# Kernel tuning notes

Measured on AMD Instinct MI355X. Metric: run time of the kernel, lower is better.

The kernel has to match this reference:

```python
import jax, jax.numpy as jnp
import numpy as np

N = 524288   # total samples
D = 128      # embedding dim
S = 128      # samples per group (equal-size contiguous groups)
G = N // S   # number of groups = 4096
MARGIN = 2.0
K_MARGIN = 0.02
EPS = 1e-6


def setup_inputs() -> dict:
    key = jax.random.key(0)
    k1, k2, k3, k4 = jax.random.split(key, 4)
    z_r = jax.random.normal(k1, (N, D), jnp.float32)
    z_v = jax.random.normal(k2, (N, D), jnp.float32)
    labels = jax.random.randint(k3, (N,), 0, 2, dtype=jnp.int32)
    # contiguous equal-size groups: group id = index // S
    groups = (jnp.arange(N, dtype=jnp.int32) // S).astype(jnp.int32)
    var_lens = jax.random.randint(k4, (N,), 0, 100, dtype=jnp.int32)
    return {"z_r": z_r, "z_v": z_v, "labels": labels, "groups": groups, "var_lens": var_lens}


def _std1(x):
    # torch.Tensor.std default is unbiased (ddof=1)
    return jnp.std(x, axis=1, ddof=1)


def reference(z_r, z_v, labels, groups, var_lens):
    # cosine distance per row: [N]
    d = 1.0 - jnp.sum(z_r * z_v, axis=-1)

    # ----- contrastive distance-difference loss -----
    mb = labels == 0
    mp = labels == 1
    nb = mb.sum()
    npos = mp.sum()
    mean_b = jnp.sum(jnp.where(mb, d, 0.0)) / jnp.maximum(nb, 1)
    mean_p = jnp.sum(jnp.where(mp, d, 0.0)) / jnp.maximum(npos, 1)
    l_cdd = jnp.where((nb > 0) & (npos > 0),
                      jax.nn.relu(MARGIN + mean_b - mean_p), 0.0)

    # ----- per-group losses, vectorized over groups as [G, S] -----
    # groups is arange(N)//S -> contiguous equal-size groups, so reshape is exact
    vlen = var_lens.reshape(G, S).astype(jnp.float32)
    dist = d.reshape(G, S)

    vs = _std1(vlen)   # [G]
    ds = _std1(dist)   # [G]
    vz = (vlen - vlen.mean(axis=1, keepdims=True)) / (vs[:, None] + EPS)
    dz = (dist - dist.mean(axis=1, keepdims=True)) / (ds[:, None] + EPS)
    corr_loss = jnp.where((vs > 0) & (ds > 0),
                          jnp.mean((vz - dz) ** 2, axis=1), 0.0)  # [G]

    order = jnp.argsort(vlen, axis=1)
    v_sorted = jnp.take_along_axis(vlen, order, axis=1)  # [G,S]
    d_sorted = jnp.take_along_axis(dist, order, axis=1)  # [G,S]

    neigh_viol = jnp.mean(
        jax.nn.relu(d_sorted[:, :-1] - d_sorted[:, 1:] + K_MARGIN), axis=1)  # [G]

    # pairwise diffs: dv[g,i,j] = v[g,j] - v[g,i] (torch unsqueeze(0)-unsqueeze(1))
    dv = v_sorted[:, None, :] - v_sorted[:, :, None]  # [G,S,S]
    dd = d_sorted[:, None, :] - d_sorted[:, :, None]  # [G,S,S]
    mask = dv > 0
    cnt = mask.sum(axis=(1, 2))  # [G]
    viol_sum = jnp.sum(jnp.where(mask, jax.nn.relu(K_MARGIN - dd), 0.0), axis=(1, 2))
    rank_loss = jnp.where(cnt > 0, viol_sum / jnp.maximum(cnt, 1), 0.0)  # [G]

    group_losses = corr_loss + neigh_viol + rank_loss  # [G]
    sizes = jnp.full((G,), float(S), jnp.float32)
    weights = sizes / sizes.sum()
    l_pcc = jnp.sum(weights * group_losses)

    return (l_cdd, l_pcc, d)
```

## Files before the change

### kernel.cpp

```cpp
#include <hip/hip_runtime.h>
#include <hip/hip_bf16.h>

#define D_DIM   128
#define S_GRP   128
#define MARGINF 2.0f
#define KMARG   0.02f
#define EPSF    1e-6f

#define CD_BLOCKS  1024
#define CD_THREADS 256
#define U_PAIRS    8

template <bool USE_PARTIALS>
__global__ __launch_bounds__(CD_THREADS) void compute_d_kernel(
    const float* __restrict__ zr, const float* __restrict__ zv,
    const int* __restrict__ labels, float* __restrict__ dout,
    float* __restrict__ partB, float* __restrict__ partP,
    int* __restrict__ pcntB, int* __restrict__ pcntP,
    double* __restrict__ wsd, int* __restrict__ wsi, int npairs)
{
    const int tid    = blockIdx.x * blockDim.x + threadIdx.x;
    const int wave   = tid >> 6;
    const int lane   = threadIdx.x & 63;
    const int nwaves = (gridDim.x * blockDim.x) >> 6;
    const int half   = lane >> 5;
    const int sub    = lane & 31;

    float accB = 0.f, accP = 0.f;
    int   cntB = 0,   cntP = 0;

    const int nchunks = npairs / U_PAIRS;

    for (int c = wave; c < nchunks; c += nwaves) {
        const int pair0 = c * U_PAIRS;
        float4 x[U_PAIRS], y[U_PAIRS];
        #pragma unroll
        for (int u = 0; u < U_PAIRS; ++u) {
            const size_t r = (size_t)(2 * (pair0 + u) + half);
            x[u] = ((const float4*)(zr + r * D_DIM))[sub];
            y[u] = ((const float4*)(zv + r * D_DIM))[sub];
        }
        float p[U_PAIRS];
        #pragma unroll
        for (int u = 0; u < U_PAIRS; ++u)
            p[u] = x[u].x * y[u].x + x[u].y * y[u].y
                 + x[u].z * y[u].z + x[u].w * y[u].w;
        #pragma unroll
        for (int off = 16; off; off >>= 1) {
            #pragma unroll
            for (int u = 0; u < U_PAIRS; ++u) p[u] += __shfl_xor(p[u], off);
        }
        if (sub == 0) {
            #pragma unroll
            for (int u = 0; u < U_PAIRS; ++u) {
                const int r = 2 * (pair0 + u) + half;
                const float dv = 1.0f - p[u];
                dout[r] = dv;
                if (labels[r] == 0) { accB += dv; cntB++; }
                else                { accP += dv; cntP++; }
            }
        }
    }

    #pragma unroll
    for (int off = 32; off; off >>= 1) {
        accB += __shfl_xor(accB, off);
        accP += __shfl_xor(accP, off);
        cntB += __shfl_xor(cntB, off);
        cntP += __shfl_xor(cntP, off);
    }
    __shared__ float sB[4], sP[4];
    __shared__ int   iB[4], iP[4];
    const int w = threadIdx.x >> 6;
    if (lane == 0) { sB[w] = accB; sP[w] = accP; iB[w] = cntB; iP[w] = cntP; }
    __syncthreads();
    if (threadIdx.x == 0) {
        const float tB = sB[0] + sB[1] + sB[2] + sB[3];
        const float tP = sP[0] + sP[1] + sP[2] + sP[3];
        const int   cB = iB[0] + iB[1] + iB[2] + iB[3];
        const int   cP = iP[0] + iP[1] + iP[2] + iP[3];
        if (USE_PARTIALS) {
            partB[blockIdx.x] = tB;
            partP[blockIdx.x] = tP;
            pcntB[blockIdx.x] = cB;
            pcntP[blockIdx.x] = cP;
        } else {
            atomicAdd(&wsd[0], (double)tB);
            atomicAdd(&wsd[1], (double)tP);
            atomicAdd(&wsi[0], cB);
            atomicAdd(&wsi[1], cP);
        }
    }
}

__device__ __forceinline__ float block_reduce_128(float x, volatile float* sh)
{
    #pragma unroll
    for (int off = 32; off; off >>= 1) x += __shfl_xor(x, off);
    __syncthreads();
    if ((threadIdx.x & 63) == 0) sh[threadIdx.x >> 6] = x;
    __syncthreads();
    return sh[0] + sh[1];
}

template <bool USE_PARTIALS>
__global__ __launch_bounds__(128) void group_kernel(
    const int* __restrict__ var_lens, const float* __restrict__ dvals,
    float* __restrict__ gl, double* __restrict__ pcc_sum)
{
    const int g = blockIdx.x;
    const int t = threadIdx.x;
    __shared__ float sv[S_GRP], sd[S_GRP], svs[S_GRP], sds[S_GRP];
    __shared__ float sred[2];

    const float v = (float)var_lens[(size_t)g * S_GRP + t];
    const float d = dvals[(size_t)g * S_GRP + t];
    sv[t] = v; sd[t] = d;

    const float mv = block_reduce_128(v, sred) * (1.0f / S_GRP);
    const float md = block_reduce_128(d, sred) * (1.0f / S_GRP);
    const float cv = v - mv, cd = d - md;

    const float ssv = block_reduce_128(cv * cv, sred);
    const float ssd = block_reduce_128(cd * cd, sred);
    const float vs  = sqrtf(ssv * (1.0f / (S_GRP - 1)));
    const float dsd = sqrtf(ssd * (1.0f / (S_GRP - 1)));

    const float vz = cv / (vs + EPSF);
    const float dz = cd / (dsd + EPSF);
    const float df = vz - dz;
    float corr = block_reduce_128(df * df, sred) * (1.0f / S_GRP);
    if (!(vs > 0.f && dsd > 0.f)) corr = 0.f;

    int rank = 0;
    #pragma unroll 8
    for (int j = 0; j < S_GRP; ++j) {
        const float vj = sv[j];
        rank += (vj < v) || (vj == v && j < t);
    }
    svs[rank] = v; sds[rank] = d;
    __syncthreads();

    float nv = 0.f;
    if (t < S_GRP - 1) nv = fmaxf(sds[t] - sds[t + 1] + KMARG, 0.f);
    const float neigh = block_reduce_128(nv, sred) * (1.0f / (S_GRP - 1));

    const float myv = svs[t], myd = sds[t];
    float viol = 0.f, cnt = 0.f;
    #pragma unroll 8
    for (int j = 0; j < S_GRP; ++j) {
        const float vj = svs[j];
        if (vj > myv) {
            cnt  += 1.f;
            viol += fmaxf(KMARG - (sds[j] - myd), 0.f);
        }
    }
    const float violT = block_reduce_128(viol, sred);
    const float cntT  = block_reduce_128(cnt,  sred);
    const float rloss = (cntT > 0.f) ? violT / cntT : 0.f;

    if (t == 0) {
        const float total = corr + neigh + rloss;
        if (USE_PARTIALS) gl[g] = total;
        else              atomicAdd(pcc_sum, (double)total);
    }
}

__global__ __launch_bounds__(256) void finalize_kernel(
    const float* __restrict__ partB, const float* __restrict__ partP,
    const int* __restrict__ pcntB, const int* __restrict__ pcntP,
    const float* __restrict__ gl, float* __restrict__ out,
    int nPart, int nGroups)
{
    double a0 = 0.0, a1 = 0.0, a2 = 0.0, a3 = 0.0, a4 = 0.0;
    for (int i = threadIdx.x; i < nPart; i += 256) {
        a0 += (double)partB[i];
        a1 += (double)partP[i];
        a2 += (double)pcntB[i];
        a3 += (double)pcntP[i];
    }
    for (int i = threadIdx.x; i < nGroups; i += 256)
        a4 += (double)gl[i];

    #pragma unroll
    for (int off = 32; off; off >>= 1) {
        a0 += __shfl_xor(a0, off);
        a1 += __shfl_xor(a1, off);
        a2 += __shfl_xor(a2, off);
        a3 += __shfl_xor(a3, off);
        a4 += __shfl_xor(a4, off);
    }
    __shared__ double red[5][4];
    const int w = threadIdx.x >> 6;
    if ((threadIdx.x & 63) == 0) {
        red[0][w] = a0; red[1][w] = a1; red[2][w] = a2; red[3][w] = a3; red[4][w] = a4;
    }
    __syncthreads();
    if (threadIdx.x == 0) {
        const double sB = red[0][0] + red[0][1] + red[0][2] + red[0][3];
        const double sP = red[1][0] + red[1][1] + red[1][2] + red[1][3];
        const double cB = red[2][0] + red[2][1] + red[2][2] + red[2][3];
        const double cP = red[3][0] + red[3][1] + red[3][2] + red[3][3];
        const double sG = red[4][0] + red[4][1] + red[4][2] + red[4][3];
        const double mean_b = sB / (cB > 0.0 ? cB : 1.0);
        const double mean_p = sP / (cP > 0.0 ? cP : 1.0);
        float l = 0.f;
        if (cB > 0.0 && cP > 0.0) {
            const double vv = (double)MARGINF + mean_b - mean_p;
            l = (float)(vv > 0.0 ? vv : 0.0);
        }
        out[0] = l;
        out[1] = (float)(sG / (double)nGroups);
    }
}

__global__ void finalize_atomic_kernel(const double* __restrict__ wsd,
                                       const int* __restrict__ wsi,
                                       float* __restrict__ out, int nGroups)
{
    if (threadIdx.x == 0 && blockIdx.x == 0) {
        const int nb = wsi[0], np_ = wsi[1];
        const double mean_b = wsd[0] / (double)(nb  > 0 ? nb  : 1);
        const double mean_p = wsd[1] / (double)(np_ > 0 ? np_ : 1);
        float l = 0.f;
        if (nb > 0 && np_ > 0) {
            const double v = (double)MARGINF + mean_b - mean_p;
            l = (float)(v > 0.0 ? v : 0.0);
        }
        out[0] = l;
        out[1] = (float)(wsd[2] / (double)nGroups);
    }
}

extern "C" void kernel_launch(void* const* d_in, const int* in_sizes, int n_in,
                              void* d_out, int out_size, void* d_ws, size_t ws_size,
                              hipStream_t stream)
{
    const float* zr       = (const float*)d_in[0];
    const float* zv       = (const float*)d_in[1];
    const int*   labels   = (const int*)d_in[2];
    const int*   var_lens = (const int*)d_in[4];
    float* out = (float*)d_out;

    const int N = in_sizes[2];
    const int G = N / S_GRP;

    const size_t need = (size_t)CD_BLOCKS * 16 + (size_t)G * 4;

    if (ws_size >= need) {
        float* partB = (float*)d_ws;
        float* partP = partB + CD_BLOCKS;
        int*   pcntB = (int*)(partP + CD_BLOCKS);
        int*   pcntP = pcntB + CD_BLOCKS;
        float* gl    = (float*)(pcntP + CD_BLOCKS);

        compute_d_kernel<true><<<CD_BLOCKS, CD_THREADS, 0, stream>>>(
            zr, zv, labels, out + 2, partB, partP, pcntB, pcntP,
            nullptr, nullptr, N / 2);
        group_kernel<true><<<G, 128, 0, stream>>>(var_lens, out + 2, gl, nullptr);
        finalize_kernel<<<1, 256, 0, stream>>>(partB, partP, pcntB, pcntP, gl,
                                               out, CD_BLOCKS, G);
    } else {
        double* wsd = (double*)d_ws;
        int*    wsi = (int*)((char*)d_ws + 3 * sizeof(double));
        hipMemsetAsync(d_ws, 0, 3 * sizeof(double) + 2 * sizeof(int), stream);

        compute_d_kernel<false><<<CD_BLOCKS, CD_THREADS, 0, stream>>>(
            zr, zv, labels, out + 2, nullptr, nullptr, nullptr, nullptr,
            wsd, wsi, N / 2);
        group_kernel<false><<<G, 128, 0, stream>>>(var_lens, out + 2, nullptr,
                                                   wsd + 2);
        finalize_atomic_kernel<<<1, 64, 0, stream>>>(wsd, wsi, out, G);
    }
}
```

Before: 552.6 us.

## Fuse distance computation into per-group kernel with double-buffered row loads

Merges the cosine-distance kernel and the per-group loss kernel into one kernel with one block per group. The block computes its 128 distances into LDS through a software-pipelined, double-buffered load of z_r/z_v rows, then runs the group statistics, and also emits per-group label sums for the contrastive loss. This removes a launch and the global write-then-reread of d between kernels. In exchange, the bandwidth-bound dot-product phase now runs with 128-thread blocks and carries the register pressure of the pipelined loads, and the finalize pass now reduces 4096 per-group partials instead of 1024 per-block ones.

After: 540.2 us. 2.2% less time.

```diff
diff --git a/kernel.cpp b/kernel.cpp
--- a/kernel.cpp
+++ b/kernel.cpp
@@ -1,5 +1,4 @@
 #include <hip/hip_runtime.h>
-#include <hip/hip_bf16.h>
 
 #define D_DIM   128
 #define S_GRP   128
@@ -7,92 +6,6 @@
 #define KMARG   0.02f
 #define EPSF    1e-6f
 
-#define CD_BLOCKS  1024
-#define CD_THREADS 256
-#define U_PAIRS    8
-
-template <bool USE_PARTIALS>
-__global__ __launch_bounds__(CD_THREADS) void compute_d_kernel(
-    const float* __restrict__ zr, const float* __restrict__ zv,
-    const int* __restrict__ labels, float* __restrict__ dout,
-    float* __restrict__ partB, float* __restrict__ partP,
-    int* __restrict__ pcntB, int* __restrict__ pcntP,
-    double* __restrict__ wsd, int* __restrict__ wsi, int npairs)
-{
-    const int tid    = blockIdx.x * blockDim.x + threadIdx.x;
-    const int wave   = tid >> 6;
-    const int lane   = threadIdx.x & 63;
-    const int nwaves = (gridDim.x * blockDim.x) >> 6;
-    const int half   = lane >> 5;
-    const int sub    = lane & 31;
-
-    float accB = 0.f, accP = 0.f;
-    int   cntB = 0,   cntP = 0;
-
-    const int nchunks = npairs / U_PAIRS;
-
-    for (int c = wave; c < nchunks; c += nwaves) {
-        const int pair0 = c * U_PAIRS;
-        float4 x[U_PAIRS], y[U_PAIRS];
-        #pragma unroll
-        for (int u = 0; u < U_PAIRS; ++u) {
-            const size_t r = (size_t)(2 * (pair0 + u) + half);
-            x[u] = ((const float4*)(zr + r * D_DIM))[sub];
-            y[u] = ((const float4*)(zv + r * D_DIM))[sub];
-        }
-        float p[U_PAIRS];
-        #pragma unroll
-        for (int u = 0; u < U_PAIRS; ++u)
-            p[u] = x[u].x * y[u].x + x[u].y * y[u].y
-                 + x[u].z * y[u].z + x[u].w * y[u].w;
-        #pragma unroll
-        for (int off = 16; off; off >>= 1) {
-            #pragma unroll
-            for (int u = 0; u < U_PAIRS; ++u) p[u] += __shfl_xor(p[u], off);
-        }
-        if (sub == 0) {
-            #pragma unroll
-            for (int u = 0; u < U_PAIRS; ++u) {
-                const int r = 2 * (pair0 + u) + half;
-                const float dv = 1.0f - p[u];
-                dout[r] = dv;
-                if (labels[r] == 0) { accB += dv; cntB++; }
-                else                { accP += dv; cntP++; }
-            }
-        }
-    }
-
-    #pragma unroll
-    for (int off = 32; off; off >>= 1) {
-        accB += __shfl_xor(accB, off);
-        accP += __shfl_xor(accP, off);
-        cntB += __shfl_xor(cntB, off);
-        cntP += __shfl_xor(cntP, off);
-    }
-    __shared__ float sB[4], sP[4];
-    __shared__ int   iB[4], iP[4];
-    const int w = threadIdx.x >> 6;
-    if (lane == 0) { sB[w] = accB; sP[w] = accP; iB[w] = cntB; iP[w] = cntP; }
-    __syncthreads();
-    if (threadIdx.x == 0) {
-        const float tB = sB[0] + sB[1] + sB[2] + sB[3];
-        const float tP = sP[0] + sP[1] + sP[2] + sP[3];
-        const int   cB = iB[0] + iB[1] + iB[2] + iB[3];
-        const int   cP = iP[0] + iP[1] + iP[2] + iP[3];
-        if (USE_PARTIALS) {
-            partB[blockIdx.x] = tB;
-            partP[blockIdx.x] = tP;
-            pcntB[blockIdx.x] = cB;
-            pcntP[blockIdx.x] = cP;
-        } else {
-            atomicAdd(&wsd[0], (double)tB);
-            atomicAdd(&wsd[1], (double)tP);
-            atomicAdd(&wsi[0], cB);
-            atomicAdd(&wsi[1], cP);
-        }
-    }
-}
-
 __device__ __forceinline__ float block_reduce_128(float x, volatile float* sh)
 {
     #pragma unroll
@@ -104,23 +17,95 @@
 }
 
 template <bool USE_PARTIALS>
-__global__ __launch_bounds__(128) void group_kernel(
-    const int* __restrict__ var_lens, const float* __restrict__ dvals,
-    float* __restrict__ gl, double* __restrict__ pcc_sum)
-{
-    const int g = blockIdx.x;
-    const int t = threadIdx.x;
-    __shared__ float sv[S_GRP], sd[S_GRP], svs[S_GRP], sds[S_GRP];
+__global__ __launch_bounds__(128, 4) void fused_kernel(
+    const float* __restrict__ zr, const float* __restrict__ zv,
+    const int* __restrict__ labels, const int* __restrict__ var_lens,
+    float* __restrict__ dout,
+    float* __restrict__ gl, float* __restrict__ pB, float* __restrict__ pP,
+    float* __restrict__ pcB, float* __restrict__ pcP,
+    double* __restrict__ wsd, int* __restrict__ wsi)
+{
+    const int g    = blockIdx.x;
+    const int t    = threadIdx.x;
+    const int w    = t >> 6;
+    const int lane = t & 63;
+    const int half = lane >> 5;
+    const int sub  = lane & 31;
+
+    __shared__ __align__(16) float sv[S_GRP], sd[S_GRP], svs[S_GRP], sds[S_GRP];
     __shared__ float sred[2];
 
-    const float v = (float)var_lens[(size_t)g * S_GRP + t];
-    const float d = dvals[(size_t)g * S_GRP + t];
-    sv[t] = v; sd[t] = d;
+    const int slabRow = g * S_GRP + w * 64;
+    const int ldsRow  = w * 64;
+
+    float4 XA[4], YA[4], XB[4], YB[4];
+
+#define LOAD8(X, Y, ls) do {                                                  \
+        const float* _bz = zr + (size_t)(slabRow + 8*(ls) + 4*half) * D_DIM;  \
+        const float* _bv = zv + (size_t)(slabRow + 8*(ls) + 4*half) * D_DIM;  \
+        _Pragma("unroll")                                                     \
+        for (int u = 0; u < 4; ++u) {                                         \
+            X[u] = ((const float4*)(_bz + (size_t)u * D_DIM))[sub];           \
+            Y[u] = ((const float4*)(_bv + (size_t)u * D_DIM))[sub];           \
+        } } while (0)
+
+#define DOT_STORE(X, Y, ls) do {                                              \
+        float _p[4];                                                          \
+        _Pragma("unroll")                                                     \
+        for (int u = 0; u < 4; ++u)                                           \
+            _p[u] = X[u].x*Y[u].x + X[u].y*Y[u].y                             \
+                  + X[u].z*Y[u].z + X[u].w*Y[u].w;                            \
+        _Pragma("unroll")                                                     \
+        for (int off = 16; off; off >>= 1) {                                  \
+            _Pragma("unroll")                                                 \
+            for (int u = 0; u < 4; ++u) _p[u] += __shfl_xor(_p[u], off);      \
+        }                                                                     \
+        if (sub == 0) {                                                       \
+            const float4 _dv = make_float4(1.f - _p[0], 1.f - _p[1],          \
+                                           1.f - _p[2], 1.f - _p[3]);         \
+                      \
+            float* _dp = dout + (size_t)(slabRow + 8*(ls)) + 4*half;          \
+            ((float2*)_dp)[0] = make_float2(_dv.x, _dv.y);                    \
+            ((float2*)_dp)[1] = make_float2(_dv.z, _dv.w);                    \
+            ((float4*)sd)[((ldsRow + 8*(ls)) >> 2) + half] = _dv;             \
+        } } while (0)
+
+    LOAD8(XA, YA, 0);
+    LOAD8(XB, YB, 1);
+    DOT_STORE(XA, YA, 0);
+    LOAD8(XA, YA, 2);
+    DOT_STORE(XB, YB, 1);
+    LOAD8(XB, YB, 3);
+    DOT_STORE(XA, YA, 2);
+    LOAD8(XA, YA, 4);
+    DOT_STORE(XB, YB, 3);
+    LOAD8(XB, YB, 5);
+    DOT_STORE(XA, YA, 4);
+    LOAD8(XA, YA, 6);
+    DOT_STORE(XB, YB, 5);
+    LOAD8(XB, YB, 7);
+    DOT_STORE(XA, YA, 6);
+    DOT_STORE(XB, YB, 7);
+
+#undef LOAD8
+#undef DOT_STORE
+
+    __syncthreads();
+
+    const float v   = (float)var_lens[(size_t)g * S_GRP + t];
+    const int   lab = labels[(size_t)g * S_GRP + t];
+    const float d   = sd[t];
+    sv[t] = v;
 
     const float mv = block_reduce_128(v, sred) * (1.0f / S_GRP);
     const float md = block_reduce_128(d, sred) * (1.0f / S_GRP);
+
+    const float sumB = block_reduce_128(lab == 0 ? d   : 0.f, sred);
+    const float cntB = block_reduce_128(lab == 0 ? 1.f : 0.f, sred);
+    const float sumP = md * (float)S_GRP - sumB;
+    const float cntP = (float)S_GRP - cntB;
+
     const float cv = v - mv, cd = d - md;
-
     const float ssv = block_reduce_128(cv * cv, sred);
     const float ssd = block_reduce_128(cd * cd, sred);
     const float vs  = sqrtf(ssv * (1.0f / (S_GRP - 1)));
@@ -161,26 +146,33 @@
 
     if (t == 0) {
         const float total = corr + neigh + rloss;
-        if (USE_PARTIALS) gl[g] = total;
-        else              atomicAdd(pcc_sum, (double)total);
+        if (USE_PARTIALS) {
+            gl[g]  = total;
+            pB[g]  = sumB; pP[g]  = sumP;
+            pcB[g] = cntB; pcP[g] = cntP;
+        } else {
+            atomicAdd(&wsd[2], (double)total);
+            atomicAdd(&wsd[0], (double)sumB);
+            atomicAdd(&wsd[1], (double)sumP);
+            atomicAdd(&wsi[0], (int)cntB);
+            atomicAdd(&wsi[1], (int)cntP);
+        }
     }
 }
 
 __global__ __launch_bounds__(256) void finalize_kernel(
-    const float* __restrict__ partB, const float* __restrict__ partP,
-    const int* __restrict__ pcntB, const int* __restrict__ pcntP,
-    const float* __restrict__ gl, float* __restrict__ out,
-    int nPart, int nGroups)
+    const float* __restrict__ pB, const float* __restrict__ pP,
+    const float* __restrict__ pcB, const float* __restrict__ pcP,
+    const float* __restrict__ gl, float* __restrict__ out, int nGroups)
 {
     double a0 = 0.0, a1 = 0.0, a2 = 0.0, a3 = 0.0, a4 = 0.0;
-    for (int i = threadIdx.x; i < nPart; i += 256) {
-        a0 += (double)partB[i];
-        a1 += (double)partP[i];
-        a2 += (double)pcntB[i];
-        a3 += (double)pcntP[i];
-    }
-    for (int i = threadIdx.x; i < nGroups; i += 256)
+    for (int i = threadIdx.x; i < nGroups; i += 256) {
+        a0 += (double)pB[i];
+        a1 += (double)pP[i];
+        a2 += (double)pcB[i];
+        a3 += (double)pcP[i];
         a4 += (double)gl[i];
+    }
 
     #pragma unroll
     for (int off = 32; off; off >>= 1) {
@@ -245,31 +237,27 @@
     const int N = in_sizes[2];
     const int G = N / S_GRP;
 
-    const size_t need = (size_t)CD_BLOCKS * 16 + (size_t)G * 4;
+    const size_t need = (size_t)G * 5 * sizeof(float);
 
     if (ws_size >= need) {
-        float* partB = (float*)d_ws;
-        float* partP = partB + CD_BLOCKS;
-        int*   pcntB = (int*)(partP + CD_BLOCKS);
-        int*   pcntP = pcntB + CD_BLOCKS;
-        float* gl    = (float*)(pcntP + CD_BLOCKS);
-
-        compute_d_kernel<true><<<CD_BLOCKS, CD_THREADS, 0, stream>>>(
-            zr, zv, labels, out + 2, partB, partP, pcntB, pcntP,
-            nullptr, nullptr, N / 2);
-        group_kernel<true><<<G, 128, 0, stream>>>(var_lens, out + 2, gl, nullptr);
-        finalize_kernel<<<1, 256, 0, stream>>>(partB, partP, pcntB, pcntP, gl,
-                                               out, CD_BLOCKS, G);
+        float* pB  = (float*)d_ws;
+        float* pP  = pB  + G;
+        float* pcB = pP  + G;
+        float* pcP = pcB + G;
+        float* gl  = pcP + G;
+
+        fused_kernel<true><<<G, 128, 0, stream>>>(
+            zr, zv, labels, var_lens, out + 2,
+            gl, pB, pP, pcB, pcP, nullptr, nullptr);
+        finalize_kernel<<<1, 256, 0, stream>>>(pB, pP, pcB, pcP, gl, out, G);
     } else {
         double* wsd = (double*)d_ws;
         int*    wsi = (int*)((char*)d_ws + 3 * sizeof(double));
         hipMemsetAsync(d_ws, 0, 3 * sizeof(double) + 2 * sizeof(int), stream);
 
-        compute_d_kernel<false><<<CD_BLOCKS, CD_THREADS, 0, stream>>>(
-            zr, zv, labels, out + 2, nullptr, nullptr, nullptr, nullptr,
-            wsd, wsi, N / 2);
-        group_kernel<false><<<G, 128, 0, stream>>>(var_lens, out + 2, nullptr,
-                                                   wsd + 2);
+        fused_kernel<false><<<G, 128, 0, stream>>>(
+            zr, zv, labels, var_lens, out + 2,
+            nullptr, nullptr, nullptr, nullptr, nullptr, wsd, wsi);
         finalize_atomic_kernel<<<1, 64, 0, stream>>>(wsd, wsi, out, G);
     }
 }
```
